# Kernel tuning notes

Measured on AMD Instinct MI355X. Metric: run time of the kernel, lower is better.

Reference implementation:

```python
import jax, jax.numpy as jnp
import numpy as np
from jax import lax

# Stacked SimpleRNN (Keras): h_t = tanh(x_t @ W + h_{t-1} @ U + b).
# Dropout(0.5) is only active in training mode; this reference implements
# inference (training=None -> dropout disabled), matching model(x).

B, T, F = 512, 512, 78
HIDDENS = (16, 32, 64, 70)
NUM_CLASSES = 5


def _glorot(key, shape):
    fan_in, fan_out = shape[0], shape[1]
    lim = float(np.sqrt(6.0 / (fan_in + fan_out)))
    return jax.random.uniform(key, shape, jnp.float32, -lim, lim)


def setup_inputs() -> dict:
    key = jax.random.key(0)
    ks = jax.random.split(key, 16)
    x = jax.random.normal(ks[0], (B, T, F), jnp.float32)
    params = {}
    in_dim = F
    for i, h in enumerate(HIDDENS):
        params[f"W{i}"] = _glorot(ks[1 + 3 * i], (in_dim, h))
        params[f"U{i}"] = _glorot(ks[2 + 3 * i], (h, h))
        params[f"b{i}"] = jnp.zeros((h,), jnp.float32)
        in_dim = h
    params["Wd"] = _glorot(ks[13], (HIDDENS[-1], NUM_CLASSES))
    params["bd"] = jnp.zeros((NUM_CLASSES,), jnp.float32)
    return {"x": x, **params}


def _simple_rnn(x, W, U, b, return_sequences):
    # Precompute input projection for all timesteps: [B, T, H]
    xw = jnp.einsum("btf,fh->bth", x, W) + b
    h0 = jnp.zeros((x.shape[0], W.shape[1]), x.dtype)

    def step(h, xw_t):
        h_new = jnp.tanh(xw_t + h @ U)
        return h_new, h_new

    h_last, hs = lax.scan(step, h0, jnp.swapaxes(xw, 0, 1))  # scan over time
    if return_sequences:
        return jnp.swapaxes(hs, 0, 1)  # [B, T, H]
    return h_last  # [B, H]


def reference(x, W0, U0, b0, W1, U1, b1, W2, U2, b2, W3, U3, b3, Wd, bd):
    h = _simple_rnn(x, W0, U0, b0, True)
    h = _simple_rnn(h, W1, U1, b1, True)
    h = _simple_rnn(h, W2, U2, b2, True)
    h = _simple_rnn(h, W3, U3, b3, False)  # [B, 70]
    logits = h @ Wd + bd  # [B, 5]
    return jax.nn.softmax(logits, axis=-1)
```

## Files before the change

### kernel.cpp

```cpp
#include <hip/hip_runtime.h>
#include <cstddef>
#include <cstdint>

#define REC_ATTR __attribute__((amdgpu_waves_per_eu(1, 1)))

#define BB 512
#define TT 512
#define M_TOTAL (BB * TT)

#define LDS_BARRIER() asm volatile("s_waitcnt lgkmcnt(0)\n\ts_barrier" ::: "memory")

__device__ __forceinline__ float tanh_fast(float x) {
  float ax = fabsf(x);
  float e = __expf(ax + ax);
  float r = 1.0f - 2.0f / (e + 1.0f);
  return (x >= 0.0f) ? r : -r;
}

__device__ __forceinline__ void fma4(float4& a, float s, const float4 w) {
  a.x = fmaf(s, w.x, a.x);
  a.y = fmaf(s, w.y, a.y);
  a.z = fmaf(s, w.z, a.z);
  a.w = fmaf(s, w.w, a.w);
}

template<int K, int N, int CG>
__global__ __launch_bounds__(256)
void proj_kernel(const float* __restrict__ in, const float* __restrict__ W,
                 const float* __restrict__ bias, float* __restrict__ out, int M)
{
  constexpr int NP = CG * 4;
  constexpr int RG = 256 / CG;
  __shared__ __align__(16) float wlds[K][NP];
  __shared__ __align__(16) float blds[NP];
  const int tid = threadIdx.x;
  for (int idx = tid; idx < K * NP; idx += 256) {
    int k = idx / NP, jj = idx - k * NP;
    wlds[k][jj] = (jj < N) ? W[k * N + jj] : 0.0f;
  }
  if (tid < NP) blds[tid] = (tid < N) ? bias[tid] : 0.0f;
  __syncthreads();

  const int c = tid % CG;
  const int rg = tid / CG;
  if (rg >= RG) return;
  const int j0 = c * 4;
  const long row0 = (long)blockIdx.x * (RG * 4) + (long)rg * 4;

  float4 b4 = *reinterpret_cast<const float4*>(&blds[j0]);
  float4 acc[4] = {b4, b4, b4, b4};
  const float* inp[4];
  bool rv[4];
  #pragma unroll
  for (int rr = 0; rr < 4; ++rr) {
    long rowi = row0 + rr;
    rv[rr] = rowi < M;
    inp[rr] = in + (rv[rr] ? rowi : 0) * (long)K;
  }

  int k = 0;
  for (; k + 4 <= K; k += 4) {
    float4 w0 = *reinterpret_cast<const float4*>(&wlds[k + 0][j0]);
    float4 w1 = *reinterpret_cast<const float4*>(&wlds[k + 1][j0]);
    float4 w2 = *reinterpret_cast<const float4*>(&wlds[k + 2][j0]);
    float4 w3 = *reinterpret_cast<const float4*>(&wlds[k + 3][j0]);
    #pragma unroll
    for (int rr = 0; rr < 4; ++rr) {
      float2 i0 = *reinterpret_cast<const float2*>(inp[rr] + k);
      float2 i1 = *reinterpret_cast<const float2*>(inp[rr] + k + 2);
      fma4(acc[rr], i0.x, w0);
      fma4(acc[rr], i0.y, w1);
      fma4(acc[rr], i1.x, w2);
      fma4(acc[rr], i1.y, w3);
    }
  }
  for (; k < K; ++k) {
    float4 w0 = *reinterpret_cast<const float4*>(&wlds[k][j0]);
    #pragma unroll
    for (int rr = 0; rr < 4; ++rr) fma4(acc[rr], inp[rr][k], w0);
  }

  #pragma unroll
  for (int rr = 0; rr < 4; ++rr) {
    if (!rv[rr]) continue;
    long obase = (row0 + rr) * (long)N + j0;
    if constexpr ((N % 4) == 0) {
      *reinterpret_cast<float4*>(&out[obase]) = acc[rr];
    } else {
      if (j0 + 4 <= N) {
        *reinterpret_cast<float2*>(&out[obase]) = make_float2(acc[rr].x, acc[rr].y);
        *reinterpret_cast<float2*>(&out[obase + 2]) = make_float2(acc[rr].z, acc[rr].w);
      } else {
        float v[4] = {acc[rr].x, acc[rr].y, acc[rr].z, acc[rr].w};
        #pragma unroll
        for (int jj = 0; jj < 4; ++jj)
          if (j0 + jj < N) out[obase + jj] = v[jj];
      }
    }
  }
}

__global__ __launch_bounds__(64) REC_ATTR
void fused_rec16(const float* __restrict__ xw, const float* __restrict__ U,
                 const float* __restrict__ Wn, const float* __restrict__ bn,
                 float* __restrict__ xwn)
{
  constexpr int H = 16, ROWS = 4, HN = 32, PF = 8;
  const int tid = threadIdx.x;
  const int r = tid >> 4, j = tid & 15;
  const int c = tid & 31, pr = tid >> 5;
  __shared__ __align__(16) float hlds[ROWS][H];
  for (int i = tid; i < ROWS * H; i += 64) reinterpret_cast<float*>(hlds)[i] = 0.0f;
  __syncthreads();

  float u[H], w[H];
  #pragma unroll
  for (int kk = 0; kk < H; ++kk) {
    u[kk] = U[kk * H + j];
    w[kk] = Wn[kk * HN + c];
    asm volatile("" : "+v"(u[kk]), "+v"(w[kk]));
  }
  const float bc = bn[c];

  const float* xwrow = xw + ((size_t)(blockIdx.x * ROWS + r) * TT) * H + j;
  float* o0 = xwn + ((size_t)(blockIdx.x * ROWS + 2 * pr + 0) * TT) * HN + c;
  float* o1 = xwn + ((size_t)(blockIdx.x * ROWS + 2 * pr + 1) * TT) * HN + c;

  float pf[PF];
  #pragma unroll
  for (int d = 0; d < PF; ++d) pf[d] = xwrow[(size_t)d * H];

  for (int t = 0; t < TT; t += PF) {
    #pragma unroll
    for (int d = 0; d < PF; ++d) {
      float xv = pf[d];
      int tn = t + d + PF;
      tn = (tn < TT) ? tn : (TT - 1);
      pf[d] = xwrow[(size_t)tn * H];

      const float* hb = &hlds[r][0];
      float a0 = xv, a1 = 0.0f, a2 = 0.0f, a3 = 0.0f;
      #pragma unroll
      for (int k4 = 0; k4 < H / 4; ++k4) {
        float4 h4 = *reinterpret_cast<const float4*>(hb + 4 * k4);
        a0 = fmaf(h4.x, u[4 * k4 + 0], a0);
        a1 = fmaf(h4.y, u[4 * k4 + 1], a1);
        a2 = fmaf(h4.z, u[4 * k4 + 2], a2);
        a3 = fmaf(h4.w, u[4 * k4 + 3], a3);
      }
      float hn = tanh_fast((a0 + a1) + (a2 + a3));
      hlds[r][j] = hn;

      const float* h0b = &hlds[2 * pr + 0][0];
      const float* h1b = &hlds[2 * pr + 1][0];
      float s0 = bc, s1 = bc, s2 = 0.0f, s3 = 0.0f;
      #pragma unroll
      for (int k4 = 0; k4 < H / 4; ++k4) {
        float4 ha = *reinterpret_cast<const float4*>(h0b + 4 * k4);
        float4 hc = *reinterpret_cast<const float4*>(h1b + 4 * k4);
        s0 = fmaf(ha.x, w[4 * k4 + 0], s0);
        s2 = fmaf(ha.y, w[4 * k4 + 1], s2);
        s0 = fmaf(ha.z, w[4 * k4 + 2], s0);
        s2 = fmaf(ha.w, w[4 * k4 + 3], s2);
        s1 = fmaf(hc.x, w[4 * k4 + 0], s1);
        s3 = fmaf(hc.y, w[4 * k4 + 1], s3);
        s1 = fmaf(hc.z, w[4 * k4 + 2], s1);
        s3 = fmaf(hc.w, w[4 * k4 + 3], s3);
      }
      o0[(size_t)(t + d) * HN] = s0 + s2;
      o1[(size_t)(t + d) * HN] = s1 + s3;
    }
  }
}

__global__ __launch_bounds__(64) REC_ATTR
void fused_rec32(const float* __restrict__ xw, const float* __restrict__ U,
                 const float* __restrict__ Wn, const float* __restrict__ bn,
                 float* __restrict__ xwn)
{
  constexpr int H = 32, ROWS = 2, HN = 64, PF = 8;
  const int tid = threadIdx.x;
  const int r = tid >> 5, j = tid & 31;
  const int c = tid;
  __shared__ __align__(16) float hlds[ROWS][H];
  for (int i = tid; i < ROWS * H; i += 64) reinterpret_cast<float*>(hlds)[i] = 0.0f;
  __syncthreads();

  float u[H], w[H];
  #pragma unroll
  for (int kk = 0; kk < H; ++kk) {
    u[kk] = U[kk * H + j];
    w[kk] = Wn[kk * HN + c];
    asm volatile("" : "+v"(u[kk]), "+v"(w[kk]));
  }
  const float bc = bn[c];

  const float* xwrow = xw + ((size_t)(blockIdx.x * ROWS + r) * TT) * H + j;
  float* o0 = xwn + ((size_t)(blockIdx.x * ROWS + 0) * TT) * HN + c;
  float* o1 = xwn + ((size_t)(blockIdx.x * ROWS + 1) * TT) * HN + c;

  float pf[PF];
  #pragma unroll
  for (int d = 0; d < PF; ++d) pf[d] = xwrow[(size_t)d * H];

  for (int t = 0; t < TT; t += PF) {
    #pragma unroll
    for (int d = 0; d < PF; ++d) {
      float xv = pf[d];
      int tn = t + d + PF;
      tn = (tn < TT) ? tn : (TT - 1);
      pf[d] = xwrow[(size_t)tn * H];

      const float* hb = &hlds[r][0];
      float a0 = xv, a1 = 0.0f, a2 = 0.0f, a3 = 0.0f;
      #pragma unroll
      for (int k4 = 0; k4 < H / 4; ++k4) {
        float4 h4 = *reinterpret_cast<const float4*>(hb + 4 * k4);
        a0 = fmaf(h4.x, u[4 * k4 + 0], a0);
        a1 = fmaf(h4.y, u[4 * k4 + 1], a1);
        a2 = fmaf(h4.z, u[4 * k4 + 2], a2);
        a3 = fmaf(h4.w, u[4 * k4 + 3], a3);
      }
      float hn = tanh_fast((a0 + a1) + (a2 + a3));
      hlds[r][j] = hn;

      const float* h0b = &hlds[0][0];
      const float* h1b = &hlds[1][0];
      float s0 = bc, s1 = bc, s2 = 0.0f, s3 = 0.0f;
      #pragma unroll
      for (int k4 = 0; k4 < H / 4; ++k4) {
        float4 ha = *reinterpret_cast<const float4*>(h0b + 4 * k4);
        float4 hc = *reinterpret_cast<const float4*>(h1b + 4 * k4);
        s0 = fmaf(ha.x, w[4 * k4 + 0], s0);
        s2 = fmaf(ha.y, w[4 * k4 + 1], s2);
        s0 = fmaf(ha.z, w[4 * k4 + 2], s0);
        s2 = fmaf(ha.w, w[4 * k4 + 3], s2);
        s1 = fmaf(hc.x, w[4 * k4 + 0], s1);
        s3 = fmaf(hc.y, w[4 * k4 + 1], s3);
        s1 = fmaf(hc.z, w[4 * k4 + 2], s1);
        s3 = fmaf(hc.w, w[4 * k4 + 3], s3);
      }
      o0[(size_t)(t + d) * HN] = s0 + s2;
      o1[(size_t)(t + d) * HN] = s1 + s3;
    }
  }
}

__global__ __launch_bounds__(64) REC_ATTR
void rec64_kernel(const float* __restrict__ xw, const float* __restrict__ U,
                  float* __restrict__ hseq)
{
  constexpr int H = 64, PF = 8;
  const int tid = threadIdx.x;
  const int row = blockIdx.x;

  __shared__ __align__(16) float hlds[H];
  hlds[tid] = 0.0f;
  __syncthreads();

  float u[H];
  #pragma unroll
  for (int kk = 0; kk < H; ++kk) {
    u[kk] = U[kk * H + tid];
    asm volatile("" : "+v"(u[kk]));
  }

  const float* xwrow = xw + ((size_t)row * TT) * H + tid;
  float* hout = hseq + ((size_t)row * TT) * H + tid;

  float pf[PF];
  #pragma unroll
  for (int d = 0; d < PF; ++d) pf[d] = xwrow[(size_t)d * H];

  for (int t = 0; t < TT; t += PF) {
    #pragma unroll
    for (int d = 0; d < PF; ++d) {
      float xv = pf[d];
      int tn = t + d + PF;
      tn = (tn < TT) ? tn : (TT - 1);
      pf[d] = xwrow[(size_t)tn * H];

      float a0 = xv, a1 = 0.0f, a2 = 0.0f, a3 = 0.0f;
      #pragma unroll
      for (int k4 = 0; k4 < H / 4; ++k4) {
        float4 h4 = *reinterpret_cast<const float4*>(&hlds[4 * k4]);
        a0 = fmaf(h4.x, u[4 * k4 + 0], a0);
        a1 = fmaf(h4.y, u[4 * k4 + 1], a1);
        a2 = fmaf(h4.z, u[4 * k4 + 2], a2);
        a3 = fmaf(h4.w, u[4 * k4 + 3], a3);
      }
      float hn = tanh_fast((a0 + a1) + (a2 + a3));
      hlds[tid] = hn;
      hout[(size_t)(t + d) * H] = hn;
    }
  }
}

__global__ __launch_bounds__(128) REC_ATTR
void rec70_kernel(const float* __restrict__ xw, const float* __restrict__ U,
                  const float* __restrict__ Wd, const float* __restrict__ bd,
                  float* __restrict__ outp)
{
  constexpr int H = 70, HP = 72, PF = 8;
  const int tid = threadIdx.x;
  const int row = blockIdx.x;
  const bool act = tid < H;
  const int j = act ? tid : 0;

  __shared__ __align__(16) float hbuf[2][HP];
  for (int i = tid; i < 2 * HP; i += 128) reinterpret_cast<float*>(hbuf)[i] = 0.0f;
  __syncthreads();

  float u[HP];
  #pragma unroll
  for (int kk = 0; kk < HP; ++kk) {
    u[kk] = (kk < H && act) ? U[kk * H + j] : 0.0f;
    asm volatile("" : "+v"(u[kk]));
  }

  const float* xwrow = xw + ((size_t)row * TT) * H + j;
  float pf[PF];
  #pragma unroll
  for (int d = 0; d < PF; ++d) pf[d] = xwrow[(size_t)d * H];

  for (int t = 0; t < TT; t += PF) {
    #pragma unroll
    for (int d = 0; d < PF; ++d) {
      float xv = pf[d];
      int tn = t + d + PF;
      tn = (tn < TT) ? tn : (TT - 1);
      pf[d] = xwrow[(size_t)tn * H];

      const float* hb = &hbuf[(t + d) & 1][0];
      float a0 = xv, a1 = 0.0f, a2 = 0.0f, a3 = 0.0f;
      #pragma unroll
      for (int k4 = 0; k4 < HP / 4; ++k4) {
        float4 h4 = *reinterpret_cast<const float4*>(hb + 4 * k4);
        a0 = fmaf(h4.x, u[4 * k4 + 0], a0);
        a1 = fmaf(h4.y, u[4 * k4 + 1], a1);
        a2 = fmaf(h4.z, u[4 * k4 + 2], a2);
        a3 = fmaf(h4.w, u[4 * k4 + 3], a3);
      }
      float hn = tanh_fast((a0 + a1) + (a2 + a3));
      if (act) hbuf[((t + d) & 1) ^ 1][j] = hn;
      LDS_BARRIER();
    }
  }

  float l = 0.0f;
  if (tid < 5) {
    l = bd[tid];
    #pragma unroll
    for (int kk = 0; kk < H; ++kk)
      l = fmaf(hbuf[0][kk], Wd[kk * 5 + tid], l);
  }
  float l0 = __shfl(l, 0), l1 = __shfl(l, 1), l2 = __shfl(l, 2),
        l3 = __shfl(l, 3), l4 = __shfl(l, 4);
  float m = fmaxf(fmaxf(fmaxf(l0, l1), fmaxf(l2, l3)), l4);
  float s = __expf(l0 - m) + __expf(l1 - m) + __expf(l2 - m) +
            __expf(l3 - m) + __expf(l4 - m);
  if (tid < 5)
    outp[(size_t)row * 5 + tid] = __expf(l - m) / s;
}

extern "C" void kernel_launch(void* const* d_in, const int* in_sizes, int n_in,
                              void* d_out, int out_size, void* d_ws, size_t ws_size,
                              hipStream_t stream)
{
  const float* x  = (const float*)d_in[0];
  const float* W0 = (const float*)d_in[1];
  const float* U0 = (const float*)d_in[2];
  const float* b0 = (const float*)d_in[3];
  const float* W1 = (const float*)d_in[4];
  const float* U1 = (const float*)d_in[5];
  const float* b1 = (const float*)d_in[6];
  const float* W2 = (const float*)d_in[7];
  const float* U2 = (const float*)d_in[8];
  const float* b2 = (const float*)d_in[9];
  const float* W3 = (const float*)d_in[10];
  const float* U3 = (const float*)d_in[11];
  const float* b3 = (const float*)d_in[12];
  const float* Wd = (const float*)d_in[13];
  const float* bd = (const float*)d_in[14];
  float* outp = (float*)d_out;

  float* A  = (float*)d_ws;
  float* Bv = (float*)((char*)d_ws + 73400320);

  const int M = M_TOTAL;

  proj_kernel<78, 16, 4><<<M / 256, 256, 0, stream>>>(x, W0, b0, A, M);
  fused_rec16<<<BB / 4, 64, 0, stream>>>(A, U0, W1, b1, Bv);
  fused_rec32<<<BB / 2, 64, 0, stream>>>(Bv, U1, W2, b2, A);
  rec64_kernel<<<BB, 64, 0, stream>>>(A, U2, Bv);
  proj_kernel<64, 70, 18><<<(M + 55) / 56, 256, 0, stream>>>(Bv, W3, b3, A, M);
  rec70_kernel<<<BB, 128, 0, stream>>>(A, U3, Wd, bd, outp);
}
```

Baseline: 990.2 us.

## Stage recurrent kernel inputs and outputs through double-buffered LDS chunks

Each recurrent kernel now loads 16-timestep slabs of the input projection with coalesced float4 global loads into a double-buffered shared-memory buffer. It also collects outputs for the chunk in shared memory and writes them back as coalesced float4 slabs. This takes per-timestep strided global loads and stores out of the serial recurrence loop, so each step only does shared-memory accesses. The cost is extra shared memory and register pressure for the next-chunk prefetch. For the single-wave kernels it also relies on in-wave ordering rather than explicit barriers.

```diff
diff --git a/kernel.cpp b/kernel.cpp
--- a/kernel.cpp
+++ b/kernel.cpp
@@ -105,13 +105,14 @@
                  const float* __restrict__ Wn, const float* __restrict__ bn,
                  float* __restrict__ xwn)
 {
-  constexpr int H = 16, ROWS = 4, HN = 32, PF = 8;
+  constexpr int H = 16, ROWS = 4, HN = 32, CH = 16, NCH = TT / CH;
+  constexpr int XINR = 264;
   const int tid = threadIdx.x;
   const int r = tid >> 4, j = tid & 15;
   const int c = tid & 31, pr = tid >> 5;
+  __shared__ __align__(16) float xin[2][ROWS * XINR];
+  __shared__ __align__(16) float xout[ROWS * CH * HN];
   __shared__ __align__(16) float hlds[ROWS][H];
-  for (int i = tid; i < ROWS * H; i += 64) reinterpret_cast<float*>(hlds)[i] = 0.0f;
-  __syncthreads();
 
   float u[H], w[H];
   #pragma unroll
@@ -122,24 +123,34 @@
   }
   const float bc = bn[c];
 
-  const float* xwrow = xw + ((size_t)(blockIdx.x * ROWS + r) * TT) * H + j;
-  float* o0 = xwn + ((size_t)(blockIdx.x * ROWS + 2 * pr + 0) * TT) * HN + c;
-  float* o1 = xwn + ((size_t)(blockIdx.x * ROWS + 2 * pr + 1) * TT) * HN + c;
-
-  float pf[PF];
-  #pragma unroll
-  for (int d = 0; d < PF; ++d) pf[d] = xwrow[(size_t)d * H];
-
-  for (int t = 0; t < TT; t += PF) {
-    #pragma unroll
-    for (int d = 0; d < PF; ++d) {
-      float xv = pf[d];
-      int tn = t + d + PF;
-      tn = (tn < TT) ? tn : (TT - 1);
-      pf[d] = xwrow[(size_t)tn * H];
-
+  const int row0 = blockIdx.x * ROWS;
+  const float* gin[ROWS];
+  float* gout[ROWS];
+  #pragma unroll
+  for (int rr = 0; rr < ROWS; ++rr) {
+    gin[rr] = xw + ((size_t)(row0 + rr) * TT) * H;
+    gout[rr] = xwn + ((size_t)(row0 + rr) * TT) * HN;
+  }
+  for (int i = tid; i < ROWS * H; i += 64) reinterpret_cast<float*>(hlds)[i] = 0.0f;
+  #pragma unroll
+  for (int rr = 0; rr < ROWS; ++rr) {
+    float4 v = reinterpret_cast<const float4*>(gin[rr])[tid];
+    *reinterpret_cast<float4*>(&xin[0][rr * XINR + tid * 4]) = v;
+  }
+
+  for (int ch = 0; ch < NCH; ++ch) {
+    const int buf = ch & 1, nb = buf ^ 1;
+    const int ch1 = (ch + 1 < NCH) ? ch + 1 : ch;
+    float4 nv[ROWS];
+    #pragma unroll
+    for (int rr = 0; rr < ROWS; ++rr)
+      nv[rr] = reinterpret_cast<const float4*>(gin[rr] + (size_t)ch1 * CH * H)[tid];
+
+    #pragma unroll
+    for (int s = 0; s < CH; ++s) {
+      float xv = xin[buf][r * XINR + s * H + j];
+      float a0 = xv, a1 = 0.0f, a2 = 0.0f, a3 = 0.0f;
       const float* hb = &hlds[r][0];
-      float a0 = xv, a1 = 0.0f, a2 = 0.0f, a3 = 0.0f;
       #pragma unroll
       for (int k4 = 0; k4 < H / 4; ++k4) {
         float4 h4 = *reinterpret_cast<const float4*>(hb + 4 * k4);
@@ -150,7 +161,6 @@
       }
       float hn = tanh_fast((a0 + a1) + (a2 + a3));
       hlds[r][j] = hn;
-
       const float* h0b = &hlds[2 * pr + 0][0];
       const float* h1b = &hlds[2 * pr + 1][0];
       float s0 = bc, s1 = bc, s2 = 0.0f, s3 = 0.0f;
@@ -167,9 +177,21 @@
         s1 = fmaf(hc.z, w[4 * k4 + 2], s1);
         s3 = fmaf(hc.w, w[4 * k4 + 3], s3);
       }
-      o0[(size_t)(t + d) * HN] = s0 + s2;
-      o1[(size_t)(t + d) * HN] = s1 + s3;
-    }
+      xout[(2 * pr + 0) * (CH * HN) + s * HN + c] = s0 + s2;
+      xout[(2 * pr + 1) * (CH * HN) + s * HN + c] = s1 + s3;
+    }
+    #pragma unroll
+    for (int rr = 0; rr < ROWS; ++rr) {
+      float* gslab = gout[rr] + (size_t)(ch * CH) * HN;
+      #pragma unroll
+      for (int q = 0; q < 2; ++q) {
+        float4 f = reinterpret_cast<const float4*>(&xout[rr * (CH * HN)])[q * 64 + tid];
+        reinterpret_cast<float4*>(gslab)[q * 64 + tid] = f;
+      }
+    }
+    #pragma unroll
+    for (int rr = 0; rr < ROWS; ++rr)
+      *reinterpret_cast<float4*>(&xin[nb][rr * XINR + tid * 4]) = nv[rr];
   }
 }
 
@@ -178,13 +200,14 @@
                  const float* __restrict__ Wn, const float* __restrict__ bn,
                  float* __restrict__ xwn)
 {
-  constexpr int H = 32, ROWS = 2, HN = 64, PF = 8;
+  constexpr int H = 32, ROWS = 2, HN = 64, CH = 16, NCH = TT / CH;
+  constexpr int XINR = 520;
   const int tid = threadIdx.x;
   const int r = tid >> 5, j = tid & 31;
   const int c = tid;
+  __shared__ __align__(16) float xin[2][ROWS * XINR];
+  __shared__ __align__(16) float xout[ROWS * CH * HN];
   __shared__ __align__(16) float hlds[ROWS][H];
-  for (int i = tid; i < ROWS * H; i += 64) reinterpret_cast<float*>(hlds)[i] = 0.0f;
-  __syncthreads();
 
   float u[H], w[H];
   #pragma unroll
@@ -195,24 +218,38 @@
   }
   const float bc = bn[c];
 
-  const float* xwrow = xw + ((size_t)(blockIdx.x * ROWS + r) * TT) * H + j;
-  float* o0 = xwn + ((size_t)(blockIdx.x * ROWS + 0) * TT) * HN + c;
-  float* o1 = xwn + ((size_t)(blockIdx.x * ROWS + 1) * TT) * HN + c;
-
-  float pf[PF];
-  #pragma unroll
-  for (int d = 0; d < PF; ++d) pf[d] = xwrow[(size_t)d * H];
-
-  for (int t = 0; t < TT; t += PF) {
-    #pragma unroll
-    for (int d = 0; d < PF; ++d) {
-      float xv = pf[d];
-      int tn = t + d + PF;
-      tn = (tn < TT) ? tn : (TT - 1);
-      pf[d] = xwrow[(size_t)tn * H];
-
+  const int row0 = blockIdx.x * ROWS;
+  const float* gin[ROWS];
+  float* gout[ROWS];
+  #pragma unroll
+  for (int rr = 0; rr < ROWS; ++rr) {
+    gin[rr] = xw + ((size_t)(row0 + rr) * TT) * H;
+    gout[rr] = xwn + ((size_t)(row0 + rr) * TT) * HN;
+  }
+  for (int i = tid; i < ROWS * H; i += 64) reinterpret_cast<float*>(hlds)[i] = 0.0f;
+  #pragma unroll
+  for (int rr = 0; rr < ROWS; ++rr)
+    #pragma unroll
+    for (int q = 0; q < 2; ++q) {
+      float4 v = reinterpret_cast<const float4*>(gin[rr])[q * 64 + tid];
+      *reinterpret_cast<float4*>(&xin[0][rr * XINR + (q * 64 + tid) * 4]) = v;
+    }
+
+  for (int ch = 0; ch < NCH; ++ch) {
+    const int buf = ch & 1, nb = buf ^ 1;
+    const int ch1 = (ch + 1 < NCH) ? ch + 1 : ch;
+    float4 nv[ROWS][2];
+    #pragma unroll
+    for (int rr = 0; rr < ROWS; ++rr)
+      #pragma unroll
+      for (int q = 0; q < 2; ++q)
+        nv[rr][q] = reinterpret_cast<const float4*>(gin[rr] + (size_t)ch1 * CH * H)[q * 64 + tid];
+
+    #pragma unroll
+    for (int s = 0; s < CH; ++s) {
+      float xv = xin[buf][r * XINR + s * H + j];
+      float a0 = xv, a1 = 0.0f, a2 = 0.0f, a3 = 0.0f;
       const float* hb = &hlds[r][0];
-      float a0 = xv, a1 = 0.0f, a2 = 0.0f, a3 = 0.0f;
       #pragma unroll
       for (int k4 = 0; k4 < H / 4; ++k4) {
         float4 h4 = *reinterpret_cast<const float4*>(hb + 4 * k4);
@@ -223,7 +260,6 @@
       }
       float hn = tanh_fast((a0 + a1) + (a2 + a3));
       hlds[r][j] = hn;
-
       const float* h0b = &hlds[0][0];
       const float* h1b = &hlds[1][0];
       float s0 = bc, s1 = bc, s2 = 0.0f, s3 = 0.0f;
@@ -240,9 +276,23 @@
         s1 = fmaf(hc.z, w[4 * k4 + 2], s1);
         s3 = fmaf(hc.w, w[4 * k4 + 3], s3);
       }
-      o0[(size_t)(t + d) * HN] = s0 + s2;
-      o1[(size_t)(t + d) * HN] = s1 + s3;
-    }
+      xout[0 * (CH * HN) + s * HN + c] = s0 + s2;
+      xout[1 * (CH * HN) + s * HN + c] = s1 + s3;
+    }
+    #pragma unroll
+    for (int rr = 0; rr < ROWS; ++rr) {
+      float* gslab = gout[rr] + (size_t)(ch * CH) * HN;
+      #pragma unroll
+      for (int q = 0; q < 4; ++q) {
+        float4 f = reinterpret_cast<const float4*>(&xout[rr * (CH * HN)])[q * 64 + tid];
+        reinterpret_cast<float4*>(gslab)[q * 64 + tid] = f;
+      }
+    }
+    #pragma unroll
+    for (int rr = 0; rr < ROWS; ++rr)
+      #pragma unroll
+      for (int q = 0; q < 2; ++q)
+        *reinterpret_cast<float4*>(&xin[nb][rr * XINR + (q * 64 + tid) * 4]) = nv[rr][q];
   }
 }
 
@@ -250,13 +300,12 @@
 void rec64_kernel(const float* __restrict__ xw, const float* __restrict__ U,
                   float* __restrict__ hseq)
 {
-  constexpr int H = 64, PF = 8;
+  constexpr int H = 64, CH = 16, NCH = TT / CH;
   const int tid = threadIdx.x;
   const int row = blockIdx.x;
-
+  __shared__ __align__(16) float xin[2][CH * H];
+  __shared__ __align__(16) float xout[CH * H];
   __shared__ __align__(16) float hlds[H];
-  hlds[tid] = 0.0f;
-  __syncthreads();
 
   float u[H];
   #pragma unroll
@@ -264,22 +313,27 @@
     u[kk] = U[kk * H + tid];
     asm volatile("" : "+v"(u[kk]));
   }
-
-  const float* xwrow = xw + ((size_t)row * TT) * H + tid;
-  float* hout = hseq + ((size_t)row * TT) * H + tid;
-
-  float pf[PF];
-  #pragma unroll
-  for (int d = 0; d < PF; ++d) pf[d] = xwrow[(size_t)d * H];
-
-  for (int t = 0; t < TT; t += PF) {
-    #pragma unroll
-    for (int d = 0; d < PF; ++d) {
-      float xv = pf[d];
-      int tn = t + d + PF;
-      tn = (tn < TT) ? tn : (TT - 1);
-      pf[d] = xwrow[(size_t)tn * H];
-
+  const float* gin = xw + ((size_t)row * TT) * H;
+  float* gout = hseq + ((size_t)row * TT) * H;
+
+  hlds[tid] = 0.0f;
+  #pragma unroll
+  for (int q = 0; q < 4; ++q) {
+    float4 v = reinterpret_cast<const float4*>(gin)[q * 64 + tid];
+    *reinterpret_cast<float4*>(&xin[0][(q * 64 + tid) * 4]) = v;
+  }
+
+  for (int ch = 0; ch < NCH; ++ch) {
+    const int buf = ch & 1, nb = buf ^ 1;
+    const int ch1 = (ch + 1 < NCH) ? ch + 1 : ch;
+    float4 nv[4];
+    #pragma unroll
+    for (int q = 0; q < 4; ++q)
+      nv[q] = reinterpret_cast<const float4*>(gin + (size_t)ch1 * CH * H)[q * 64 + tid];
+
+    #pragma unroll
+    for (int s = 0; s < CH; ++s) {
+      float xv = xin[buf][s * H + tid];
       float a0 = xv, a1 = 0.0f, a2 = 0.0f, a3 = 0.0f;
       #pragma unroll
       for (int k4 = 0; k4 < H / 4; ++k4) {
@@ -291,8 +345,17 @@
       }
       float hn = tanh_fast((a0 + a1) + (a2 + a3));
       hlds[tid] = hn;
-      hout[(size_t)(t + d) * H] = hn;
-    }
+      xout[s * H + tid] = hn;
+    }
+    float* gslab = gout + (size_t)(ch * CH) * H;
+    #pragma unroll
+    for (int q = 0; q < 4; ++q) {
+      float4 f = reinterpret_cast<const float4*>(xout)[q * 64 + tid];
+      reinterpret_cast<float4*>(gslab)[q * 64 + tid] = f;
+    }
+    #pragma unroll
+    for (int q = 0; q < 4; ++q)
+      *reinterpret_cast<float4*>(&xin[nb][(q * 64 + tid) * 4]) = nv[q];
   }
 }
 
@@ -301,15 +364,15 @@
                   const float* __restrict__ Wd, const float* __restrict__ bd,
                   float* __restrict__ outp)
 {
-  constexpr int H = 70, HP = 72, PF = 8;
+  constexpr int H = 70, HP = 72, CH = 16, NCH = TT / CH, SLAB = CH * H;
+  constexpr int NL = 9;
   const int tid = threadIdx.x;
   const int row = blockIdx.x;
   const bool act = tid < H;
   const int j = act ? tid : 0;
 
+  __shared__ __align__(16) float xin[2][1152];
   __shared__ __align__(16) float hbuf[2][HP];
-  for (int i = tid; i < 2 * HP; i += 128) reinterpret_cast<float*>(hbuf)[i] = 0.0f;
-  __syncthreads();
 
   float u[HP];
   #pragma unroll
@@ -318,20 +381,30 @@
     asm volatile("" : "+v"(u[kk]));
   }
 
-  const float* xwrow = xw + ((size_t)row * TT) * H + j;
-  float pf[PF];
-  #pragma unroll
-  for (int d = 0; d < PF; ++d) pf[d] = xwrow[(size_t)d * H];
-
-  for (int t = 0; t < TT; t += PF) {
-    #pragma unroll
-    for (int d = 0; d < PF; ++d) {
-      float xv = pf[d];
-      int tn = t + d + PF;
-      tn = (tn < TT) ? tn : (TT - 1);
-      pf[d] = xwrow[(size_t)tn * H];
-
-      const float* hb = &hbuf[(t + d) & 1][0];
+  const float* gin = xw + ((size_t)row * TT) * H;
+  for (int i = tid; i < 2 * HP; i += 128) reinterpret_cast<float*>(hbuf)[i] = 0.0f;
+  #pragma unroll
+  for (int q = 0; q < NL; ++q) {
+    int idx = q * 128 + tid;
+    xin[0][idx] = (idx < SLAB) ? gin[idx] : 0.0f;
+  }
+  __syncthreads();
+
+  for (int ch = 0; ch < NCH; ++ch) {
+    const int buf = ch & 1, nb = buf ^ 1;
+    const int ch1 = (ch + 1 < NCH) ? ch + 1 : ch;
+    const float* gslab = gin + (size_t)ch1 * SLAB;
+    float nv[NL];
+    #pragma unroll
+    for (int q = 0; q < NL; ++q) {
+      int idx = q * 128 + tid;
+      nv[q] = (idx < SLAB) ? gslab[idx] : 0.0f;
+    }
+
+    #pragma unroll
+    for (int s = 0; s < CH; ++s) {
+      float xv = xin[buf][s * H + j];
+      const float* hb = &hbuf[s & 1][0];
       float a0 = xv, a1 = 0.0f, a2 = 0.0f, a3 = 0.0f;
       #pragma unroll
       for (int k4 = 0; k4 < HP / 4; ++k4) {
@@ -342,7 +415,11 @@
         a3 = fmaf(h4.w, u[4 * k4 + 3], a3);
       }
       float hn = tanh_fast((a0 + a1) + (a2 + a3));
-      if (act) hbuf[((t + d) & 1) ^ 1][j] = hn;
+      if (act) hbuf[(s & 1) ^ 1][j] = hn;
+      if (s == CH - 1) {
+        #pragma unroll
+        for (int q = 0; q < NL; ++q) xin[nb][q * 128 + tid] = nv[q];
+      }
       LDS_BARRIER();
     }
   }
```

Result: no change. 979.9 us (-1.0%).
